# Performance work log

Hardware: AMD Instinct MI355X
Metric: run time of the kernel (lower is better)

The kernel has to match this reference:

```python
import jax, jax.numpy as jnp
import numpy as np


def _maxpool2(t):
    # 2x2 max pool, stride 2. t: [B, C, H, W]
    B, C, H, W = t.shape
    return t.reshape(B, C, H // 2, 2, W // 2, 2).max(axis=(3, 5))


def setup_inputs() -> dict:
    key = jax.random.key(0)
    ks = jax.random.split(key, 5)
    B, C, H, W = 4, 64, 128, 128
    x = jax.random.normal(ks[0], (B, C, H, W), dtype=jnp.float32)
    w_theta = jax.random.normal(ks[1], (C // 8, C), dtype=jnp.float32) * (1.0 / np.sqrt(C))
    w_phi = jax.random.normal(ks[2], (C // 8, C), dtype=jnp.float32) * (1.0 / np.sqrt(C))
    w_g = jax.random.normal(ks[3], (C // 2, C), dtype=jnp.float32) * (1.0 / np.sqrt(C))
    w_o = jax.random.normal(ks[4], (C, C // 2), dtype=jnp.float32) * (1.0 / np.sqrt(C // 2))
    gamma = jnp.ones((1,), dtype=jnp.float32)
    return {"x": x, "w_theta": w_theta, "w_phi": w_phi, "w_g": w_g, "w_o": w_o, "gamma": gamma}


def reference(x, w_theta, w_phi, w_g, w_o, gamma):
    B, C, H, W = x.shape
    N = H * W
    # 1x1 convs (bias-free) are channel matmuls
    theta = jnp.einsum('oc,bchw->bohw', w_theta, x)            # [B, C/8, H, W]
    phi = _maxpool2(jnp.einsum('oc,bchw->bohw', w_phi, x))     # [B, C/8, H/2, W/2]
    g = _maxpool2(jnp.einsum('oc,bchw->bohw', w_g, x))         # [B, C/2, H/2, W/2]
    theta = theta.reshape(B, C // 8, N)                        # [B, C/8, N]
    phi = phi.reshape(B, C // 8, N // 4)                       # [B, C/8, N/4]
    g = g.reshape(B, C // 2, N // 4)                           # [B, C/2, N/4]
    # attention: no 1/sqrt(d) scaling in SAGAN
    scores = jnp.einsum('bcn,bcm->bnm', theta, phi)            # [B, N, N/4]
    beta = jax.nn.softmax(scores, axis=-1)
    attn = jnp.einsum('bcm,bnm->bcn', g, beta)                 # [B, C/2, N]
    o = jnp.einsum('oc,bcn->bon', w_o, attn).reshape(B, C, H, W)
    return gamma[0] * o + x
```

## Files before the change

### kernel.cpp

```cpp
#include <hip/hip_runtime.h>
#include <hip/hip_bf16.h>


typedef __attribute__((ext_vector_type(4))) float f32x4;
typedef __attribute__((ext_vector_type(8))) short s16x8;
typedef __attribute__((ext_vector_type(4))) short s16x4;

__device__ __forceinline__ unsigned short f32_bf16(float f) {
    unsigned int u = __float_as_uint(f);
    return (unsigned short)((u + 0x7fffu + ((u >> 16) & 1u)) >> 16);
}
__device__ __forceinline__ unsigned int pk_bf16(float a, float b) {
    return (unsigned int)f32_bf16(a) | ((unsigned int)f32_bf16(b) << 16);
}
__device__ __forceinline__ unsigned int pk_rh(float a, float b) {
    unsigned int au = __float_as_uint(a) + 0x8000u;
    unsigned int bu = __float_as_uint(b) + 0x8000u;
    return __builtin_amdgcn_perm(bu, au, 0x07060302u);
}
__device__ __forceinline__ unsigned int pk_tr(float a, float b) {
    return __builtin_amdgcn_perm(__float_as_uint(b), __float_as_uint(a), 0x07060302u);
}
__device__ __forceinline__ void async16(const void* g, void* l) {
    __builtin_amdgcn_global_load_lds(
        (const __attribute__((address_space(1))) unsigned int*)g,
        (__attribute__((address_space(3))) unsigned int*)l, 16, 0, 0);
}

__global__ __launch_bounds__(256) void proj_kernel(
    const float* __restrict__ x,
    const float* __restrict__ w_theta, const float* __restrict__ w_phi,
    const float* __restrict__ w_g,
    __hip_bfloat16* __restrict__ thG,
    __hip_bfloat16* __restrict__ phG,
    __hip_bfloat16* __restrict__ gG)
{
    __shared__ __align__(16) unsigned short x_s[128 * 72];
    int tid = threadIdx.x;
    int bx = blockIdx.x;
    int b = bx >> 7, mh = (bx >> 1) & 63, ph = bx & 1;

    {
        int cp = tid >> 3, s = tid & 7;
        const float* xb = x + ((size_t)b << 20) + (size_t)(2 * mh) * 128 + 64 * ph;
        const float* p0r = xb + ((size_t)(2 * cp) << 14);
        const float* p1r = p0r + (1 << 14);
#pragma unroll
        for (int py = 0; py < 2; py++)
#pragma unroll
            for (int t = 0; t < 2; t++) {
                int pxl = 4 * s + 32 * t;
                float4 a = *(const float4*)(p0r + py * 128 + pxl);
                float4 c = *(const float4*)(p1r + py * 128 + pxl);
                int pix = py * 64 + pxl;
                *(unsigned int*)&x_s[(pix + 0) * 72 + 2 * cp] = pk_rh(a.x, c.x);
                *(unsigned int*)&x_s[(pix + 1) * 72 + 2 * cp] = pk_rh(a.y, c.y);
                *(unsigned int*)&x_s[(pix + 2) * 72 + 2 * cp] = pk_rh(a.z, c.z);
                *(unsigned int*)&x_s[(pix + 3) * 72 + 2 * cp] = pk_rh(a.w, c.w);
            }
    }

    int lane = tid & 63, w = tid >> 6;
    int q = lane >> 4, nl = lane & 15;

    s16x8 A[3][2];
#pragma unroll
    for (int CT = 0; CT < 3; CT++) {
        const float* wsrc;
        float scale = 1.0f;
        if (CT == 0) {
            if (nl < 8) { wsrc = w_theta + nl * 64; scale = 1.44269504f; }
            else        { wsrc = w_phi + (nl - 8) * 64; }
        } else if (CT == 1) wsrc = w_g + nl * 64;
        else                wsrc = w_g + (16 + nl) * 64;
#pragma unroll
        for (int ks = 0; ks < 2; ks++) {
            const float4* p4 = (const float4*)(wsrc + 32 * ks + 8 * q);
            float4 a0 = p4[0], a1 = p4[1];
            s16x8 f;
            f[0] = (short)f32_bf16(a0.x * scale); f[1] = (short)f32_bf16(a0.y * scale);
            f[2] = (short)f32_bf16(a0.z * scale); f[3] = (short)f32_bf16(a0.w * scale);
            f[4] = (short)f32_bf16(a1.x * scale); f[5] = (short)f32_bf16(a1.y * scale);
            f[6] = (short)f32_bf16(a1.z * scale); f[7] = (short)f32_bf16(a1.w * scale);
            A[CT][ks] = f;
        }
    }
    __syncthreads();

    f32x4 acc[3][2];
#pragma unroll
    for (int ti = 0; ti < 2; ti++) {
        int tile = w + 4 * ti;
        const unsigned short* rb = x_s + (16 * tile + nl) * 72;
        s16x8 B0 = *(const s16x8*)(rb + 8 * q);
        s16x8 B1 = *(const s16x8*)(rb + 32 + 8 * q);
#pragma unroll
        for (int CT = 0; CT < 3; CT++) {
            f32x4 d = (f32x4){0.f, 0.f, 0.f, 0.f};
            d = __builtin_amdgcn_mfma_f32_16x16x32_bf16(A[CT][0], B0, d, 0, 0, 0);
            d = __builtin_amdgcn_mfma_f32_16x16x32_bf16(A[CT][1], B1, d, 0, 0, 0);
            acc[CT][ti] = d;
        }
    }

    if (q < 2) {
        unsigned short* thb = (unsigned short*)thG + ((size_t)b << 14) * 8;
#pragma unroll
        for (int ti = 0; ti < 2; ti++) {
            int n = (2 * mh + ti) * 128 + 64 * ph + 16 * w + nl;
            uint2 tv;
            tv.x = pk_bf16(acc[0][ti][0], acc[0][ti][1]);
            tv.y = pk_bf16(acc[0][ti][2], acc[0][ti][3]);
            *(uint2*)(thb + (size_t)n * 8 + 4 * q) = tv;
        }
    }

    float pool[3][4];
#pragma unroll
    for (int CT = 0; CT < 3; CT++)
#pragma unroll
        for (int r = 0; r < 4; r++) {
            float a = fmaxf(acc[CT][0][r], acc[CT][1][r]);
            pool[CT][r] = fmaxf(a, __shfl_xor(a, 1));
        }

    int mm = 8 * w + (nl >> 1);
    int mbase = mh * 64 + ph * 32;
    if ((nl & 1) == 0) {
        if (q >= 2) {
            uint2 pv;
            pv.x = pk_bf16(pool[0][0], pool[0][1]);
            pv.y = pk_bf16(pool[0][2], pool[0][3]);
            *(uint2*)((unsigned short*)phG + ((size_t)(b * 4096 + mbase + mm)) * 8 + (q - 2) * 4) = pv;
        }
        int p = 8 * ((mm >> 2) & 3) + 4 * ((mm >> 4) & 1) + (mm & 3);
        int mstore = mbase + p;
#pragma unroll
        for (int CT = 1; CT < 3; CT++)
#pragma unroll
            for (int r = 0; r < 4; r++) {
                int cg = 16 * (CT - 1) + 4 * q + r;
                ((unsigned short*)gG)[((size_t)(b * 32 + cg) << 12) + mstore] =
                    f32_bf16(pool[CT][r]);
            }
    }
}

__global__ __launch_bounds__(512) void attn_kernel(
    const __hip_bfloat16* __restrict__ thG, const __hip_bfloat16* __restrict__ phG,
    const __hip_bfloat16* __restrict__ gG,
    const float* __restrict__ w_o, const float* __restrict__ gamma,
    const float* __restrict__ x, float* __restrict__ out)
{
    __shared__ __align__(16) unsigned char smem[2 * 16384 + 2 * 4096];
    unsigned char* O_s = smem;

    int tid = threadIdx.x, lane = tid & 63, w = tid >> 6;
    int q = lane >> 4, nl = lane & 15;
    int bx = blockIdx.x;
    int b  = bx >> 7;
    int n0 = (bx & 127) << 7;
    int nw = n0 + w * 16;

    const unsigned short* thb = (const unsigned short*)thG + ((size_t)b << 14) * 8;
    const unsigned short* phb = (const unsigned short*)phG + ((size_t)b << 12) * 8;
    const unsigned short* ggb = (const unsigned short*)gG + ((size_t)b << 17);

    s16x8 BT = (s16x8){0, 0, 0, 0, 0, 0, 0, 0};
    if (q == 0)      BT = *(const s16x8*)(thb + (size_t)(nw + nl) * 8);
    else if (q == 1) BT[0] = (short)0xC167;
    s16x8 Fc = (s16x8){0, 0, 0, 0, 0, 0, 0, 0};
    if (q == 1) Fc[0] = (short)0x3F80;

    f32x4 acc0 = (f32x4){0.f, 0.f, 0.f, 0.f};
    f32x4 acc1 = (f32x4){0.f, 0.f, 0.f, 0.f};
    float l = 0.f;

    int crow0 = 2 * w + (lane >> 5);
    int crow1 = crow0 + 16;
    const unsigned short* gsrc0 = ggb + ((size_t)crow0 << 12) + 8 * ((lane & 31) ^ crow0);
    const unsigned short* gsrc1 = ggb + ((size_t)crow1 << 12) + 8 * ((lane & 31) ^ crow1);
    const unsigned short* psrc  = phb + (size_t)((w & 3) * 64 + lane) * 8;
    unsigned char* ldsg0 = smem + w * 1024;
    unsigned char* ldsg1 = smem + 8192 + w * 1024;
    unsigned char* ldsp  = smem + 32768 + (w & 3) * 1024;

    async16(gsrc0, ldsg0);
    async16(gsrc1, ldsg1);
    if (w < 4) async16(psrc, ldsp);
    __syncthreads();

    for (int st = 0; st < 16; st++) {
        const unsigned char* gcur = smem + (st & 1) * 16384;
        const unsigned char* pcur = smem + 32768 + (st & 1) * 4096;
        if (st < 15) {
            int mo = (st + 1) << 8;
            int nb = (st + 1) & 1;
            async16(gsrc0 + mo, ldsg0 + nb * 16384);
            async16(gsrc1 + mo, ldsg1 + nb * 16384);
            if (w < 4) async16(psrc + (size_t)mo * 8, ldsp + nb * 4096);
        }
#pragma unroll
        for (int cc = 0; cc < 8; cc++) {
            int mloc = cc << 5;
            s16x8 F0 = Fc, F1 = Fc;
            if (q == 0) {
                F0 = *(const s16x8*)(pcur + (mloc + nl) * 16);
                F1 = *(const s16x8*)(pcur + (mloc + 16 + nl) * 16);
            }
            f32x4 z = (f32x4){0.f, 0.f, 0.f, 0.f};
            f32x4 sc0 = __builtin_amdgcn_mfma_f32_16x16x32_bf16(F0, BT, z, 0, 0, 0);
            f32x4 sc1 = __builtin_amdgcn_mfma_f32_16x16x32_bf16(F1, BT, z, 0, 0, 0);
            float e0 = __builtin_amdgcn_exp2f(sc0[0]);
            float e1 = __builtin_amdgcn_exp2f(sc0[1]);
            float e2 = __builtin_amdgcn_exp2f(sc0[2]);
            float e3 = __builtin_amdgcn_exp2f(sc0[3]);
            float f0 = __builtin_amdgcn_exp2f(sc1[0]);
            float f1 = __builtin_amdgcn_exp2f(sc1[1]);
            float f2 = __builtin_amdgcn_exp2f(sc1[2]);
            float f3 = __builtin_amdgcn_exp2f(sc1[3]);
            l += ((e0 + e1) + (e2 + e3)) + ((f0 + f1) + (f2 + f3));
            uint2 u0 = make_uint2(pk_tr(e0, e1), pk_tr(e2, e3));
            uint2 u1 = make_uint2(pk_tr(f0, f1), pk_tr(f2, f3));
            s16x4 P0 = *(s16x4*)&u0;
            s16x4 P1 = *(s16x4*)&u1;
            int t = (cc << 2) + q;
            s16x8 G0 = *(const s16x8*)(gcur + nl * 512 + ((t ^ nl) << 4));
            s16x8 G1 = *(const s16x8*)(gcur + (nl + 16) * 512 + ((t ^ (nl + 16)) << 4));
            s16x4 G0a = __builtin_shufflevector(G0, G0, 0, 1, 2, 3);
            s16x4 G0b = __builtin_shufflevector(G0, G0, 4, 5, 6, 7);
            s16x4 G1a = __builtin_shufflevector(G1, G1, 0, 1, 2, 3);
            s16x4 G1b = __builtin_shufflevector(G1, G1, 4, 5, 6, 7);
            acc0 = __builtin_amdgcn_mfma_f32_16x16x16bf16_1k(G0a, P0, acc0, 0, 0, 0);
            acc0 = __builtin_amdgcn_mfma_f32_16x16x16bf16_1k(G0b, P1, acc0, 0, 0, 0);
            acc1 = __builtin_amdgcn_mfma_f32_16x16x16bf16_1k(G1a, P0, acc1, 0, 0, 0);
            acc1 = __builtin_amdgcn_mfma_f32_16x16x16bf16_1k(G1b, P1, acc1, 0, 0, 0);
        }
        __syncthreads();
    }

    l += __shfl_xor(l, 16);
    l += __shfl_xor(l, 32);
    float linv = 1.0f / l;
    acc0 *= linv;
    acc1 *= linv;

    s16x8 WO[4];
#pragma unroll
    for (int g4 = 0; g4 < 4; g4++) {
        const float4* wr = (const float4*)(w_o + (size_t)(g4 * 16 + nl) * 32 + q * 8);
        float4 a0 = wr[0], a1 = wr[1];
        WO[g4][0] = (short)f32_bf16(a0.x); WO[g4][1] = (short)f32_bf16(a0.y);
        WO[g4][2] = (short)f32_bf16(a0.z); WO[g4][3] = (short)f32_bf16(a0.w);
        WO[g4][4] = (short)f32_bf16(a1.x); WO[g4][5] = (short)f32_bf16(a1.y);
        WO[g4][6] = (short)f32_bf16(a1.z); WO[g4][7] = (short)f32_bf16(a1.w);
    }
    float gam = gamma[0];

    int n_loc = w * 16 + nl;
    {
        uint2 ov;
        ov.x = pk_bf16(acc0[0], acc0[1]);
        ov.y = pk_bf16(acc0[2], acc0[3]);
        *(uint2*)(O_s + n_loc * 80 + q * 8) = ov;
        ov.x = pk_bf16(acc1[0], acc1[1]);
        ov.y = pk_bf16(acc1[2], acc1[3]);
        *(uint2*)(O_s + n_loc * 80 + 32 + q * 8) = ov;
    }
    s16x8 OB = *(const s16x8*)(O_s + n_loc * 80 + q * 16);
#pragma unroll
    for (int g4 = 0; g4 < 4; g4++) {
        f32x4 d = (f32x4){0.f, 0.f, 0.f, 0.f};
        d = __builtin_amdgcn_mfma_f32_16x16x32_bf16(WO[g4], OB, d, 0, 0, 0);
#pragma unroll
        for (int r = 0; r < 4; r++) {
            int cc = g4 * 16 + q * 4 + r;
            size_t gi = (((size_t)(b * 64 + cc)) << 14) + nw + nl;
            out[gi] = gam * d[r] + x[gi];
        }
    }
}

extern "C" void kernel_launch(void* const* d_in, const int* in_sizes, int n_in,
                              void* d_out, int out_size, void* d_ws, size_t ws_size,
                              hipStream_t stream) {
    const float* x       = (const float*)d_in[0];
    const float* w_theta = (const float*)d_in[1];
    const float* w_phi   = (const float*)d_in[2];
    const float* w_g     = (const float*)d_in[3];
    const float* w_o     = (const float*)d_in[4];
    const float* gamma   = (const float*)d_in[5];
    float* out = (float*)d_out;

    __hip_bfloat16* thG = (__hip_bfloat16*)d_ws;
    __hip_bfloat16* phG = thG + 524288;
    __hip_bfloat16* gG  = phG + 131072;

    proj_kernel<<<512, 256, 0, stream>>>(x, w_theta, w_phi, w_g, thG, phG, gG);
    attn_kernel<<<512, 512, 0, stream>>>(thG, phG, gG, w_o, gamma, x, out);
}
```

Baseline: 129.9 us.

## Give each attention wavefront two query tiles and sum softmax denominators with MFMA

```diff
diff --git a/kernel.cpp b/kernel.cpp
--- a/kernel.cpp
+++ b/kernel.cpp
@@ -146,7 +146,7 @@
     }
 }
 
-__global__ __launch_bounds__(512) void attn_kernel(
+__global__ __launch_bounds__(256) void attn_kernel(
     const __hip_bfloat16* __restrict__ thG, const __hip_bfloat16* __restrict__ phG,
     const __hip_bfloat16* __restrict__ gG,
     const float* __restrict__ w_o, const float* __restrict__ gamma,
@@ -160,34 +160,49 @@
     int bx = blockIdx.x;
     int b  = bx >> 7;
     int n0 = (bx & 127) << 7;
-    int nw = n0 + w * 16;
+    int nw = n0 + w * 32;
 
     const unsigned short* thb = (const unsigned short*)thG + ((size_t)b << 14) * 8;
     const unsigned short* phb = (const unsigned short*)phG + ((size_t)b << 12) * 8;
     const unsigned short* ggb = (const unsigned short*)gG + ((size_t)b << 17);
 
-    s16x8 BT = (s16x8){0, 0, 0, 0, 0, 0, 0, 0};
-    if (q == 0)      BT = *(const s16x8*)(thb + (size_t)(nw + nl) * 8);
-    else if (q == 1) BT[0] = (short)0xC167;
+    s16x8 BT0 = (s16x8){0, 0, 0, 0, 0, 0, 0, 0};
+    s16x8 BT1 = (s16x8){0, 0, 0, 0, 0, 0, 0, 0};
+    if (q == 0) {
+        BT0 = *(const s16x8*)(thb + (size_t)(nw + nl) * 8);
+        BT1 = *(const s16x8*)(thb + (size_t)(nw + 16 + nl) * 8);
+    } else if (q == 1) {
+        BT0[0] = (short)0xC167;
+        BT1[0] = (short)0xC167;
+    }
     s16x8 Fc = (s16x8){0, 0, 0, 0, 0, 0, 0, 0};
     if (q == 1) Fc[0] = (short)0x3F80;
-
-    f32x4 acc0 = (f32x4){0.f, 0.f, 0.f, 0.f};
-    f32x4 acc1 = (f32x4){0.f, 0.f, 0.f, 0.f};
-    float l = 0.f;
-
-    int crow0 = 2 * w + (lane >> 5);
-    int crow1 = crow0 + 16;
-    const unsigned short* gsrc0 = ggb + ((size_t)crow0 << 12) + 8 * ((lane & 31) ^ crow0);
-    const unsigned short* gsrc1 = ggb + ((size_t)crow1 << 12) + 8 * ((lane & 31) ^ crow1);
-    const unsigned short* psrc  = phb + (size_t)((w & 3) * 64 + lane) * 8;
-    unsigned char* ldsg0 = smem + w * 1024;
-    unsigned char* ldsg1 = smem + 8192 + w * 1024;
-    unsigned char* ldsp  = smem + 32768 + (w & 3) * 1024;
+    const s16x4 ONE4 = (s16x4){(short)0x3F80, (short)0x3F80, (short)0x3F80, (short)0x3F80};
+
+    f32x4 acc00 = (f32x4){0.f, 0.f, 0.f, 0.f};
+    f32x4 acc10 = (f32x4){0.f, 0.f, 0.f, 0.f};
+    f32x4 acc01 = (f32x4){0.f, 0.f, 0.f, 0.f};
+    f32x4 acc11 = (f32x4){0.f, 0.f, 0.f, 0.f};
+    f32x4 accL0 = (f32x4){0.f, 0.f, 0.f, 0.f};
+    f32x4 accL1 = (f32x4){0.f, 0.f, 0.f, 0.f};
+
+    int r0 = 8 * w + (lane >> 5);
+    const unsigned short* gsrc0 = ggb + ((size_t)(r0 + 0) << 12) + 8 * ((lane & 31) ^ (r0 + 0));
+    const unsigned short* gsrc1 = ggb + ((size_t)(r0 + 2) << 12) + 8 * ((lane & 31) ^ (r0 + 2));
+    const unsigned short* gsrc2 = ggb + ((size_t)(r0 + 4) << 12) + 8 * ((lane & 31) ^ (r0 + 4));
+    const unsigned short* gsrc3 = ggb + ((size_t)(r0 + 6) << 12) + 8 * ((lane & 31) ^ (r0 + 6));
+    const unsigned short* psrc  = phb + (size_t)(w * 64 + lane) * 8;
+    unsigned char* ldsg0 = smem + w * 4096;
+    unsigned char* ldsg1 = ldsg0 + 1024;
+    unsigned char* ldsg2 = ldsg0 + 2048;
+    unsigned char* ldsg3 = ldsg0 + 3072;
+    unsigned char* ldsp  = smem + 32768 + w * 1024;
 
     async16(gsrc0, ldsg0);
     async16(gsrc1, ldsg1);
-    if (w < 4) async16(psrc, ldsp);
+    async16(gsrc2, ldsg2);
+    async16(gsrc3, ldsg3);
+    async16(psrc, ldsp);
     __syncthreads();
 
     for (int st = 0; st < 16; st++) {
@@ -198,7 +213,9 @@
             int nb = (st + 1) & 1;
             async16(gsrc0 + mo, ldsg0 + nb * 16384);
             async16(gsrc1 + mo, ldsg1 + nb * 16384);
-            if (w < 4) async16(psrc + (size_t)mo * 8, ldsp + nb * 4096);
+            async16(gsrc2 + mo, ldsg2 + nb * 16384);
+            async16(gsrc3 + mo, ldsg3 + nb * 16384);
+            async16(psrc + (size_t)mo * 8, ldsp + nb * 4096);
         }
 #pragma unroll
         for (int cc = 0; cc < 8; cc++) {
@@ -208,42 +225,67 @@
                 F0 = *(const s16x8*)(pcur + (mloc + nl) * 16);
                 F1 = *(const s16x8*)(pcur + (mloc + 16 + nl) * 16);
             }
-            f32x4 z = (f32x4){0.f, 0.f, 0.f, 0.f};
-            f32x4 sc0 = __builtin_amdgcn_mfma_f32_16x16x32_bf16(F0, BT, z, 0, 0, 0);
-            f32x4 sc1 = __builtin_amdgcn_mfma_f32_16x16x32_bf16(F1, BT, z, 0, 0, 0);
-            float e0 = __builtin_amdgcn_exp2f(sc0[0]);
-            float e1 = __builtin_amdgcn_exp2f(sc0[1]);
-            float e2 = __builtin_amdgcn_exp2f(sc0[2]);
-            float e3 = __builtin_amdgcn_exp2f(sc0[3]);
-            float f0 = __builtin_amdgcn_exp2f(sc1[0]);
-            float f1 = __builtin_amdgcn_exp2f(sc1[1]);
-            float f2 = __builtin_amdgcn_exp2f(sc1[2]);
-            float f3 = __builtin_amdgcn_exp2f(sc1[3]);
-            l += ((e0 + e1) + (e2 + e3)) + ((f0 + f1) + (f2 + f3));
-            uint2 u0 = make_uint2(pk_tr(e0, e1), pk_tr(e2, e3));
-            uint2 u1 = make_uint2(pk_tr(f0, f1), pk_tr(f2, f3));
-            s16x4 P0 = *(s16x4*)&u0;
-            s16x4 P1 = *(s16x4*)&u1;
             int t = (cc << 2) + q;
             s16x8 G0 = *(const s16x8*)(gcur + nl * 512 + ((t ^ nl) << 4));
             s16x8 G1 = *(const s16x8*)(gcur + (nl + 16) * 512 + ((t ^ (nl + 16)) << 4));
+
+            f32x4 z = (f32x4){0.f, 0.f, 0.f, 0.f};
+            f32x4 s00 = __builtin_amdgcn_mfma_f32_16x16x32_bf16(F0, BT0, z, 0, 0, 0);
+            f32x4 s01 = __builtin_amdgcn_mfma_f32_16x16x32_bf16(F1, BT0, z, 0, 0, 0);
+            f32x4 s10 = __builtin_amdgcn_mfma_f32_16x16x32_bf16(F0, BT1, z, 0, 0, 0);
+            f32x4 s11 = __builtin_amdgcn_mfma_f32_16x16x32_bf16(F1, BT1, z, 0, 0, 0);
+
+            float a0 = __builtin_amdgcn_exp2f(s00[0]);
+            float a1 = __builtin_amdgcn_exp2f(s00[1]);
+            float a2 = __builtin_amdgcn_exp2f(s00[2]);
+            float a3 = __builtin_amdgcn_exp2f(s00[3]);
+            float b0 = __builtin_amdgcn_exp2f(s01[0]);
+            float b1 = __builtin_amdgcn_exp2f(s01[1]);
+            float b2 = __builtin_amdgcn_exp2f(s01[2]);
+            float b3 = __builtin_amdgcn_exp2f(s01[3]);
+            float c0 = __builtin_amdgcn_exp2f(s10[0]);
+            float c1 = __builtin_amdgcn_exp2f(s10[1]);
+            float c2 = __builtin_amdgcn_exp2f(s10[2]);
+            float c3 = __builtin_amdgcn_exp2f(s10[3]);
+            float d0 = __builtin_amdgcn_exp2f(s11[0]);
+            float d1 = __builtin_amdgcn_exp2f(s11[1]);
+            float d2 = __builtin_amdgcn_exp2f(s11[2]);
+            float d3 = __builtin_amdgcn_exp2f(s11[3]);
+
+            uint2 u00 = make_uint2(pk_tr(a0, a1), pk_tr(a2, a3));
+            uint2 u01 = make_uint2(pk_tr(b0, b1), pk_tr(b2, b3));
+            uint2 u10 = make_uint2(pk_tr(c0, c1), pk_tr(c2, c3));
+            uint2 u11 = make_uint2(pk_tr(d0, d1), pk_tr(d2, d3));
+            s16x4 P00 = *(s16x4*)&u00;
+            s16x4 P01 = *(s16x4*)&u01;
+            s16x4 P10 = *(s16x4*)&u10;
+            s16x4 P11 = *(s16x4*)&u11;
+
+            accL0 = __builtin_amdgcn_mfma_f32_16x16x16bf16_1k(ONE4, P00, accL0, 0, 0, 0);
+            accL0 = __builtin_amdgcn_mfma_f32_16x16x16bf16_1k(ONE4, P01, accL0, 0, 0, 0);
+            accL1 = __builtin_amdgcn_mfma_f32_16x16x16bf16_1k(ONE4, P10, accL1, 0, 0, 0);
+            accL1 = __builtin_amdgcn_mfma_f32_16x16x16bf16_1k(ONE4, P11, accL1, 0, 0, 0);
+
             s16x4 G0a = __builtin_shufflevector(G0, G0, 0, 1, 2, 3);
             s16x4 G0b = __builtin_shufflevector(G0, G0, 4, 5, 6, 7);
             s16x4 G1a = __builtin_shufflevector(G1, G1, 0, 1, 2, 3);
             s16x4 G1b = __builtin_shufflevector(G1, G1, 4, 5, 6, 7);
-            acc0 = __builtin_amdgcn_mfma_f32_16x16x16bf16_1k(G0a, P0, acc0, 0, 0, 0);
-            acc0 = __builtin_amdgcn_mfma_f32_16x16x16bf16_1k(G0b, P1, acc0, 0, 0, 0);
-            acc1 = __builtin_amdgcn_mfma_f32_16x16x16bf16_1k(G1a, P0, acc1, 0, 0, 0);
-            acc1 = __builtin_amdgcn_mfma_f32_16x16x16bf16_1k(G1b, P1, acc1, 0, 0, 0);
+            acc00 = __builtin_amdgcn_mfma_f32_16x16x16bf16_1k(G0a, P00, acc00, 0, 0, 0);
+            acc00 = __builtin_amdgcn_mfma_f32_16x16x16bf16_1k(G0b, P01, acc00, 0, 0, 0);
+            acc10 = __builtin_amdgcn_mfma_f32_16x16x16bf16_1k(G1a, P00, acc10, 0, 0, 0);
+            acc10 = __builtin_amdgcn_mfma_f32_16x16x16bf16_1k(G1b, P01, acc10, 0, 0, 0);
+            acc01 = __builtin_amdgcn_mfma_f32_16x16x16bf16_1k(G0a, P10, acc01, 0, 0, 0);
+            acc01 = __builtin_amdgcn_mfma_f32_16x16x16bf16_1k(G0b, P11, acc01, 0, 0, 0);
+            acc11 = __builtin_amdgcn_mfma_f32_16x16x16bf16_1k(G1a, P10, acc11, 0, 0, 0);
+            acc11 = __builtin_amdgcn_mfma_f32_16x16x16bf16_1k(G1b, P11, acc11, 0, 0, 0);
         }
         __syncthreads();
     }
 
-    l += __shfl_xor(l, 16);
-    l += __shfl_xor(l, 32);
-    float linv = 1.0f / l;
-    acc0 *= linv;
-    acc1 *= linv;
+    float li0 = 1.0f / accL0[0];
+    float li1 = 1.0f / accL1[0];
+    acc00 *= li0; acc10 *= li0;
+    acc01 *= li1; acc11 *= li1;
 
     s16x8 WO[4];
 #pragma unroll
@@ -257,26 +299,34 @@
     }
     float gam = gamma[0];
 
-    int n_loc = w * 16 + nl;
+    int nloc0 = w * 32 + nl;
+    int nloc1 = nloc0 + 16;
     {
         uint2 ov;
-        ov.x = pk_bf16(acc0[0], acc0[1]);
-        ov.y = pk_bf16(acc0[2], acc0[3]);
-        *(uint2*)(O_s + n_loc * 80 + q * 8) = ov;
-        ov.x = pk_bf16(acc1[0], acc1[1]);
-        ov.y = pk_bf16(acc1[2], acc1[3]);
-        *(uint2*)(O_s + n_loc * 80 + 32 + q * 8) = ov;
-    }
-    s16x8 OB = *(const s16x8*)(O_s + n_loc * 80 + q * 16);
+        ov.x = pk_bf16(acc00[0], acc00[1]); ov.y = pk_bf16(acc00[2], acc00[3]);
+        *(uint2*)(O_s + nloc0 * 80 + q * 8) = ov;
+        ov.x = pk_bf16(acc10[0], acc10[1]); ov.y = pk_bf16(acc10[2], acc10[3]);
+        *(uint2*)(O_s + nloc0 * 80 + 32 + q * 8) = ov;
+        ov.x = pk_bf16(acc01[0], acc01[1]); ov.y = pk_bf16(acc01[2], acc01[3]);
+        *(uint2*)(O_s + nloc1 * 80 + q * 8) = ov;
+        ov.x = pk_bf16(acc11[0], acc11[1]); ov.y = pk_bf16(acc11[2], acc11[3]);
+        *(uint2*)(O_s + nloc1 * 80 + 32 + q * 8) = ov;
+    }
+    s16x8 OB0 = *(const s16x8*)(O_s + nloc0 * 80 + q * 16);
+    s16x8 OB1 = *(const s16x8*)(O_s + nloc1 * 80 + q * 16);
 #pragma unroll
     for (int g4 = 0; g4 < 4; g4++) {
-        f32x4 d = (f32x4){0.f, 0.f, 0.f, 0.f};
-        d = __builtin_amdgcn_mfma_f32_16x16x32_bf16(WO[g4], OB, d, 0, 0, 0);
+        f32x4 e0 = (f32x4){0.f, 0.f, 0.f, 0.f};
+        f32x4 e1 = (f32x4){0.f, 0.f, 0.f, 0.f};
+        e0 = __builtin_amdgcn_mfma_f32_16x16x32_bf16(WO[g4], OB0, e0, 0, 0, 0);
+        e1 = __builtin_amdgcn_mfma_f32_16x16x32_bf16(WO[g4], OB1, e1, 0, 0, 0);
 #pragma unroll
         for (int r = 0; r < 4; r++) {
             int cc = g4 * 16 + q * 4 + r;
-            size_t gi = (((size_t)(b * 64 + cc)) << 14) + nw + nl;
-            out[gi] = gam * d[r] + x[gi];
+            size_t gi0 = (((size_t)(b * 64 + cc)) << 14) + nw + nl;
+            out[gi0] = gam * e0[r] + x[gi0];
+            size_t gi1 = gi0 + 16;
+            out[gi1] = gam * e1[r] + x[gi1];
         }
     }
 }
@@ -297,5 +347,5 @@
     __hip_bfloat16* gG  = phG + 131072;
 
     proj_kernel<<<512, 256, 0, stream>>>(x, w_theta, w_phi, w_g, thG, phG, gG);
-    attn_kernel<<<512, 512, 0, stream>>>(thG, phG, gG, w_o, gamma, x, out);
-}
+    attn_kernel<<<512, 256, 0, stream>>>(thG, phG, gG, w_o, gamma, x, out);
+}
```

New measurement: 137.1 us. 1.06x slower.
